# Kernel tuning notes

Hardware: AMD Instinct MI355X
Metric: run time of the kernel (lower is better)

The kernel has to match this reference:

```python
import jax, jax.numpy as jnp
import numpy as np

B, T, V, EMB, KBD, H, NF, OUT = 256, 50, 100000, 64, 64, 128, 10, 64


def setup_inputs() -> dict:
    key = jax.random.key(0)
    ks = jax.random.split(key, 18)
    s = 0.05
    f = lambda i, shape: jax.random.normal(ks[i], shape, jnp.float32) * s
    return {
        "X": jax.random.randint(ks[0], (B, T), 0, V),
        "E": f(1, (V, EMB)),
        "KBE": f(2, (V, KBD)),
        "r_matrix": f(3, (NF, KBD)),
        "gru_Wih": f(4, (3 * H, EMB)),
        "gru_Whh": f(5, (3 * H, H)),
        "gru_bih": f(6, (3 * H,)),
        "gru_bhh": f(7, (3 * H,)),
        "u_W": f(8, (KBD, H)),
        "u_b": f(9, (KBD,)),
        "ea_W": f(10, (KBD, KBD)),
        "ea_b": f(11, (KBD,)),
        "u2_W": f(12, (H, KBD + H)),
        "u2_b": f(13, (H,)),
        "m1_W": f(14, (OUT, H)),
        "m1_b": f(15, (OUT,)),
        "m2_W": f(16, (OUT, EMB + KBD)),
        "m2_b": f(17, (OUT,)),
    }


def reference(X, E, KBE, r_matrix, gru_Wih, gru_Whh, gru_bih, gru_bhh,
              u_W, u_b, ea_W, ea_b, u2_W, u2_b, m1_W, m1_b, m2_W, m2_b):
    b, t = X.shape
    nf, d = r_matrix.shape
    hdim = gru_Whh.shape[1]
    # mask row 0 of the embedding tables (padding item)
    Em = E.at[0].set(0.0)
    KBEm = KBE.at[0].set(0.0)
    Sx = Em[X]        # [B,T,EMB]
    KBx = KBEm[X]     # [B,T,KBD]

    h0 = jnp.zeros((b, hdim), Sx.dtype)
    MN0 = jnp.zeros((b, nf, d), Sx.dtype)
    ysum0 = jnp.zeros((b, m1_b.shape[0]), Sx.dtype)

    def step(carry, xs):
        h, MN, ysum = carry
        x_emb, kb = xs
        # torch GRUCell
        gi = x_emb @ gru_Wih.T + gru_bih
        gh = h @ gru_Whh.T + gru_bhh
        ir, iz, inn = jnp.split(gi, 3, axis=1)
        hr, hz, hn = jnp.split(gh, 3, axis=1)
        r = jax.nn.sigmoid(ir + hr)
        z = jax.nn.sigmoid(iz + hz)
        n = jnp.tanh(inn + r * hn)
        h = (1.0 - z) * n + z * h
        # memory write
        EA = jnp.tanh(kb @ ea_W.T + ea_b)[:, None, :] + r_matrix      # [B,NF,D]
        gate = jax.nn.sigmoid(jnp.sum(MN * EA, axis=-1, keepdims=True))  # [B,NF,1]
        MN = MN * (1.0 - gate) + EA * gate
        # memory read
        U = jnp.tanh(h @ u_W.T + u_b)                                  # [B,D]
        AW = jax.nn.softmax(U @ r_matrix.T, axis=1)                    # [B,NF]
        AC = jnp.einsum('bnd,bn->bd', MN, AW)                          # [B,D]
        Ut = jnp.tanh(jnp.concatenate([h, AC], axis=-1) @ u2_W.T + u2_b)
        y = jnp.tanh(Ut @ m1_W.T + m1_b)                               # [B,OUT]
        return (h, MN, ysum + y), None

    (h, MN, ysum), _ = jax.lax.scan(
        step, (h0, MN0, ysum0),
        (Sx.transpose(1, 0, 2), KBx.transpose(1, 0, 2)))
    y = ysum / t

    MergeE = jnp.concatenate([E, KBE], axis=1).at[0].set(0.0)  # [V, EMB+KBD]
    Sy = jnp.tanh(MergeE @ m2_W.T + m2_b)                      # [V, OUT]
    return jax.nn.log_softmax(y @ Sy.T, axis=1)                # [B, V]
```

## Files before the change

kernel.cpp:

```cpp
#include <hip/hip_runtime.h>
#include <hip/hip_bf16.h>
#include <math.h>

#define BB 256
#define TT 50
#define VV 100000
#define EMB 64
#define KBD 64
#define HH 128
#define NF 10
#define OUTD 64
#define G3H 384
#define NTILE 6250
#define DSTR 16
#define NSY 240

typedef __attribute__((ext_vector_type(8))) short sh8;
typedef __attribute__((ext_vector_type(4))) short sh4;
typedef __attribute__((ext_vector_type(4))) float f32x4;

__device__ __forceinline__ float frcp(float x){ return __builtin_amdgcn_rcpf(x); }
__device__ __forceinline__ float sigm(float x){ return frcp(1.0f+__expf(-x)); }
__device__ __forceinline__ float tanhf_(float x){ return 1.0f - 2.0f*frcp(__expf(2.0f*x)+1.0f); }
__device__ __forceinline__ short f2bs(float f){ __hip_bfloat16 h=__float2bfloat16(f); return *reinterpret_cast<short*>(&h); }
__device__ __forceinline__ sh8 ldfrag(const float* p){
  float4 a = *(const float4*)p; float4 b = *(const float4*)(p+4);
  sh8 v;
  v[0]=f2bs(a.x); v[1]=f2bs(a.y); v[2]=f2bs(a.z); v[3]=f2bs(a.w);
  v[4]=f2bs(b.x); v[5]=f2bs(b.y); v[6]=f2bs(b.z); v[7]=f2bs(b.w);
  return v;
}
__device__ __forceinline__ void barrier_lds(){
  asm volatile("s_waitcnt lgkmcnt(0)" ::: "memory");
  __builtin_amdgcn_sched_barrier(0);
  __builtin_amdgcn_s_barrier();
  __builtin_amdgcn_sched_barrier(0);
}

__global__ void k_trans(const float* __restrict__ Wih, const float* __restrict__ eaW,
                        float* __restrict__ WihT, float* __restrict__ eaWT) {
  int stride = gridDim.x*blockDim.x;
  int tid0 = blockIdx.x*blockDim.x + threadIdx.x;
  for (int i=tid0; i<G3H*EMB; i+=stride){ int j=i/EMB, k=i%EMB; WihT[k*G3H+j]=Wih[i]; }
  for (int i=tid0; i<KBD*KBD; i+=stride){ int j=i/KBD, k=i%KBD; eaWT[k*KBD+j]=eaW[i]; }
}

#define PREP 32
__global__ __launch_bounds__(512) void k_preSy(
    const int* __restrict__ X, const float* __restrict__ E, const float* __restrict__ KBE,
    const float* __restrict__ WihT, const float* __restrict__ bih, const float* __restrict__ bhh,
    const float* __restrict__ eaWT, const float* __restrict__ eab,
    float* __restrict__ gi_pre, float* __restrict__ ea_pre,
    __hip_bfloat16* __restrict__ ea_bfT,
    const float* __restrict__ m2W, const float* __restrict__ m2b,
    __hip_bfloat16* __restrict__ Sy) {
  const int tid = threadIdx.x;
  const int w = tid>>6, l = tid&63, r16 = l&15, g4 = l>>4;

  if (blockIdx.x >= 400) {
    int kof = g4*8;
    sh8 bbf[4][4];
    float bias[4];
    #pragma unroll
    for (int nt=0;nt<4;nt++){
      int o = nt*16 + r16;
      bias[nt] = m2b[o];
      #pragma unroll
      for (int ks=0;ks<4;ks++) bbf[nt][ks] = ldfrag(m2W + o*128 + ks*32 + kof);
    }
    int wid = (blockIdx.x-400)*8 + w;
    for (int tile=wid; tile<NTILE; tile+=NSY*8){
      int v = tile*16 + r16;
      sh8 aa[4];
      const float* ep = E + (size_t)v*EMB + kof;
      const float* kp = KBE + (size_t)v*KBD + kof;
      aa[0] = ldfrag(ep); aa[1] = ldfrag(ep+32);
      aa[2] = ldfrag(kp); aa[3] = ldfrag(kp+32);
      if (v==0){ sh8 z={0,0,0,0,0,0,0,0}; aa[0]=z;aa[1]=z;aa[2]=z;aa[3]=z; }
      f32x4 acc[4];
      #pragma unroll
      for (int nt=0;nt<4;nt++){ f32x4 z={0.f,0.f,0.f,0.f}; acc[nt]=z; }
      #pragma unroll
      for (int nt=0;nt<4;nt++)
        #pragma unroll
        for (int ks=0;ks<4;ks++)
          acc[nt] = __builtin_amdgcn_mfma_f32_16x16x32_bf16(aa[ks],bbf[nt][ks],acc[nt],0,0,0);
      #pragma unroll
      for (int nt=0;nt<4;nt++){
        #pragma unroll
        for (int r=0;r<4;r++){
          int vv = tile*16 + g4*4 + r;
          Sy[(size_t)vv*OUTD + nt*16 + r16] = __float2bfloat16(tanhf_(acc[nt][r] + bias[nt]));
        }
      }
    }
    return;
  }

  __shared__ float xeL[PREP][EMB];
  __shared__ float kbL[PREP][KBD];
  int base = blockIdx.x * PREP;
  for (int i=tid; i<PREP*EMB; i+=512){
    int p=i>>6, k=i&63; int x = X[base+p];
    xeL[p][k] = x ? E[(size_t)x*EMB+k] : 0.0f;
    kbL[p][k] = x ? KBE[(size_t)x*KBD+k] : 0.0f;
  }
  __syncthreads();
  if (tid < G3H) {
    int j = tid;
    float acc[PREP];
    #pragma unroll
    for (int p=0;p<PREP;p++) acc[p]=0.f;
    for (int k=0;k<EMB;k++){
      float ww = WihT[k*G3H+j];
      #pragma unroll
      for (int p=0;p<PREP;p++) acc[p] += ww*xeL[p][k];
    }
    float bj = bih[j] + (j < 2*HH ? bhh[j] : 0.0f);
    for (int p=0;p<PREP;p++) gi_pre[((size_t)(base+p))*G3H + j] = acc[p]+bj;
  }
  {
    int d = tid & 63; int pg = tid >> 6;
    float bd = eab[d];
    for (int p=pg; p<PREP; p+=8){
      float acc=0.f;
      #pragma unroll 8
      for (int k=0;k<KBD;k++) acc += eaWT[k*KBD+d]*kbL[p][k];
      float v = tanhf(acc + bd);
      int pair = base+p;
      int bb = pair/TT, tt = pair - bb*TT;
      ea_pre[((size_t)pair)*KBD + d] = v;
      ea_bfT[((size_t)bb*64 + d)*64 + tt] = __float2bfloat16(v);
    }
  }
}

__global__ __launch_bounds__(256,2) void k_scanh(
    const float* __restrict__ gi_pre,
    const float* __restrict__ Whh, const float* __restrict__ bhh,
    const float* __restrict__ ea_pre, const float* __restrict__ rmat,
    float* __restrict__ Gg, float* __restrict__ Pg,
    __hip_bfloat16* __restrict__ h_stream) {
  const int tid = threadIdx.x;
  const int w = tid>>6, l = tid&63, r16 = l&15, g4 = l>>4;

  if (blockIdx.x >= 16) {
    const int b = (blockIdx.x-16)*4 + w;
    sh8 aa[4][2];
    #pragma unroll
    for (int i=0;i<4;i++){
      int row = i*16 + r16; if (row > TT-1) row = TT-1;
      #pragma unroll
      for (int f=0;f<2;f++)
        aa[i][f] = ldfrag(ea_pre + ((size_t)b*TT + row)*KBD + f*32 + g4*8);
    }
    sh8 rmB[2];
    #pragma unroll
    for (int f=0;f<2;f++){
      sh8 z = {0,0,0,0,0,0,0,0};
      if (r16 < NF) z = ldfrag(rmat + (size_t)r16*KBD + f*32 + g4*8);
      rmB[f] = z;
    }
    float* Gb = Gg + ((size_t)b<<12);
    #pragma unroll
    for (int i=0;i<4;i++){
      #pragma unroll
      for (int j=0;j<4;j++){
        f32x4 acc={0.f,0.f,0.f,0.f};
        #pragma unroll
        for (int f=0;f<2;f++) acc = __builtin_amdgcn_mfma_f32_16x16x32_bf16(aa[i][f], aa[j][f], acc,0,0,0);
        #pragma unroll
        for (int r=0;r<4;r++) Gb[(i*16+g4*4+r)*64 + j*16+r16] = acc[r];
      }
      f32x4 accp={0.f,0.f,0.f,0.f};
      #pragma unroll
      for (int f=0;f<2;f++) accp = __builtin_amdgcn_mfma_f32_16x16x32_bf16(aa[i][f], rmB[f], accp,0,0,0);
      #pragma unroll
      for (int r=0;r<4;r++) Pg[((size_t)b<<10) + (i*16+g4*4+r)*16 + r16] = accp[r];
    }
    return;
  }

  __shared__ __hip_bfloat16 hcat[2][16][128];
  __builtin_amdgcn_s_setprio(1);
  const int b = blockIdx.x;
  const int b0 = b*16;
  for (int i=tid;i<2*16*128;i+=256) ((short*)hcat)[i]=0;
  __syncthreads();
  const int swz = (r16&7)<<4;

  sh8 whhF[2][3][4];
  #pragma unroll
  for (int t=0;t<2;t++)
    #pragma unroll
    for (int g=0;g<3;g++){
      int chain = (w + 4*t) + 8*g;
      #pragma unroll
      for (int f=0;f<4;f++)
        whhF[t][g][f] = ldfrag(Whh + (size_t)(chain*16 + r16)*HH + f*32 + g4*8);
    }
  float4 bhn[2];
  bhn[0] = *(const float4*)(bhh + 2*HH + w*16 + g4*4);
  bhn[1] = *(const float4*)(bhh + 2*HH + (w+4)*16 + g4*4);
  float h_old[2][4] = {{0.f,0.f,0.f,0.f},{0.f,0.f,0.f,0.f}};
  const float* gi_row = gi_pre + (size_t)(b0+r16)*TT*G3H;
  __hip_bfloat16* hsb = h_stream + (size_t)b*TT*16*HH;

  int cur = 0;
  auto stepfn = [&](int s, float4 (&gi)[2][3], int cu){
    const char* hrow = (const char*)&hcat[cu][r16][0];
    sh8 hb[4];
    #pragma unroll
    for (int f=0;f<4;f++)
      hb[f] = *(const sh8*)(hrow + ((f*64 + g4*16) ^ swz));
    f32x4 aR[2], aZ[2], aN[2];
    #pragma unroll
    for (int t=0;t<2;t++){ f32x4 z={0.f,0.f,0.f,0.f}; aR[t]=z; aZ[t]=z; aN[t]=z; }
    #pragma unroll
    for (int f=0;f<4;f++){
      #pragma unroll
      for (int t=0;t<2;t++){
        aR[t] = __builtin_amdgcn_mfma_f32_16x16x32_bf16(whhF[t][0][f], hb[f], aR[t],0,0,0);
        aZ[t] = __builtin_amdgcn_mfma_f32_16x16x32_bf16(whhF[t][1][f], hb[f], aZ[t],0,0,0);
        aN[t] = __builtin_amdgcn_mfma_f32_16x16x32_bf16(whhF[t][2][f], hb[f], aN[t],0,0,0);
      }
    }
    char* hwrow = (char*)&hcat[cu^1][r16][0];
    #pragma unroll
    for (int t=0;t<2;t++){
      sh4 hp;
      #pragma unroll
      for (int r=0;r<4;r++){
        float rr = sigm(gi[t][0][r] + aR[t][r]);
        float zz = sigm(gi[t][1][r] + aZ[t][r]);
        float nn = tanhf_(gi[t][2][r] + rr*(aN[t][r] + bhn[t][r]));
        h_old[t][r] = (1.f-zz)*nn + zz*h_old[t][r];
        hp[r] = f2bs(h_old[t][r]);
      }
      *(sh4*)(hwrow + (((w+4*t)*32 + g4*8) ^ swz)) = hp;
      *(sh4*)(hsb + ((size_t)s*16 + r16)*HH + (w+4*t)*16 + g4*4) = hp;
    }
    barrier_lds();
  };

  float4 gA[2][3], gB[2][3];
  #pragma unroll
  for (int t=0;t<2;t++)
    #pragma unroll
    for (int g=0;g<3;g++)
      gA[t][g] = *(const float4*)(gi_row + g*128 + (w+4*t)*16 + g4*4);

  for (int s=0;s<TT;s+=2){
    {
      int sg = s+1;
      #pragma unroll
      for (int t=0;t<2;t++)
        #pragma unroll
        for (int g=0;g<3;g++)
          gB[t][g] = *(const float4*)(gi_row + (size_t)sg*G3H + g*128 + (w+4*t)*16 + g4*4);
      stepfn(s, gA, cur);
      cur ^= 1;
    }
    {
      int sg = (s+2<TT)? s+2 : TT-1;
      #pragma unroll
      for (int t=0;t<2;t++)
        #pragma unroll
        for (int g=0;g<3;g++)
          gA[t][g] = *(const float4*)(gi_row + (size_t)sg*G3H + g*128 + (w+4*t)*16 + g4*4);
      stepfn(s+1, gB, cur);
      cur ^= 1;
    }
  }
}

__global__ __launch_bounds__(512) void k_uaw(
    const __hip_bfloat16* __restrict__ h_stream,
    const float* __restrict__ uW, const float* __restrict__ ub,
    const float* __restrict__ rmat, float* __restrict__ aw_pre) {
  __shared__ __hip_bfloat16 u_sh[8][16][72];
  const int tid = threadIdx.x;
  const int w = tid>>6, l = tid&63, r16 = l&15, g4 = l>>4;
  sh8 uwF[4][4];
  #pragma unroll
  for (int ot=0;ot<4;ot++)
    #pragma unroll
    for (int f=0;f<4;f++)
      uwF[ot][f] = ldfrag(uW + (size_t)(ot*16+r16)*HH + f*32 + g4*8);
  sh8 rmF[2];
  #pragma unroll
  for (int f=0;f<2;f++){
    sh8 z = {0,0,0,0,0,0,0,0};
    if (r16 < NF) z = ldfrag(rmat + (size_t)r16*KBD + f*32 + g4*8);
    rmF[f] = z;
  }
  float4 ubv[4];
  #pragma unroll
  for (int ot=0;ot<4;ot++) ubv[ot] = *(const float4*)(ub + ot*16 + g4*4);

  int p0 = (blockIdx.x*8 + w)*16;
  int t = p0>>8, b0 = p0&255, fb = b0>>4;
  const __hip_bfloat16* hp = h_stream + (size_t)((fb*TT + t)*16)*HH;
  sh8 hb[4];
  #pragma unroll
  for (int f=0;f<4;f++) hb[f] = *(const sh8*)(hp + r16*HH + f*32 + g4*8);
  f32x4 u[4];
  #pragma unroll
  for (int ot=0;ot<4;ot++){ f32x4 z={0.f,0.f,0.f,0.f}; u[ot]=z; }
  #pragma unroll
  for (int ot=0;ot<4;ot++)
    #pragma unroll
    for (int f=0;f<4;f++)
      u[ot] = __builtin_amdgcn_mfma_f32_16x16x32_bf16(uwF[ot][f], hb[f], u[ot],0,0,0);
  #pragma unroll
  for (int ot=0;ot<4;ot++){
    sh4 up;
    #pragma unroll
    for (int r=0;r<4;r++) up[r] = f2bs(tanhf_(u[ot][r] + ubv[ot][r]));
    *(sh4*)&u_sh[w][l&15][ot*16 + g4*4] = up;
  }
  __syncthreads();
  sh8 uf[2];
  #pragma unroll
  for (int f=0;f<2;f++) uf[f] = *(const sh8*)&u_sh[w][r16][f*32 + g4*8];
  f32x4 al={0.f,0.f,0.f,0.f};
  #pragma unroll
  for (int f=0;f<2;f++) al = __builtin_amdgcn_mfma_f32_16x16x32_bf16(rmF[f], uf[f], al,0,0,0);
  float mx = -1e30f;
  #pragma unroll
  for (int r=0;r<4;r++){ if (g4*4+r < NF) mx = fmaxf(mx, al[r]); }
  mx = fmaxf(mx, __shfl_xor(mx,16));
  mx = fmaxf(mx, __shfl_xor(mx,32));
  float av[4]; float ssum=0.f;
  #pragma unroll
  for (int r=0;r<4;r++){ av[r] = (g4*4+r < NF) ? __expf(al[r]-mx) : 0.f; ssum += av[r]; }
  ssum += __shfl_xor(ssum,16); ssum += __shfl_xor(ssum,32);
  float inv = frcp(ssum);
  if (g4<3){
    f32x4 o = {av[0]*inv, av[1]*inv, av[2]*inv, av[3]*inv};
    *(f32x4*)&aw_pre[(size_t)(p0+r16)*16 + g4*4] = o;
  }
}

__global__ __launch_bounds__(640) void k_mnrec(
    const float* __restrict__ Gg, const float* __restrict__ Pg,
    const float* __restrict__ rmat, const float* __restrict__ aw_pre,
    __hip_bfloat16* __restrict__ Aag_bf, __hip_bfloat16* __restrict__ Bag_bf) {
  __shared__ float AagL[TT*52];
  __shared__ float BagL[TT*16];
  const int tid = threadIdx.x;
  const int n = tid>>6, l = tid&63;
  const int b = blockIdx.x;
  for (int i=tid;i<TT*52;i+=640) AagL[i]=0.f;
  for (int i=tid;i<TT*16;i+=640) BagL[i]=0.f;

  float rv = rmat[n*KBD + l];
  float R = rv*rv;
  R += __shfl_xor(R,1); R += __shfl_xor(R,2); R += __shfl_xor(R,4);
  R += __shfl_xor(R,8); R += __shfl_xor(R,16); R += __shfl_xor(R,32);

  float Pn = (l<TT)? Pg[((size_t)b<<10) + l*16 + n] : 0.f;
  const float* Gb = Gg + ((size_t)b<<12);
  float Grow = Gb[l];
  float awt = aw_pre[(size_t)(0*256+b)*16 + n];
  float d=0.f, w=0.f, q=1.f;
  __syncthreads();

  for (int t=0;t<TT;t++){
    int tn = (t+1<TT)? t+1 : TT-1;
    float GrowN = Gb[tn*64 + l];
    float awtN  = aw_pre[(size_t)(tn*256+b)*16 + n];
    float dt = __shfl(d, t);
    float g  = sigm(dt);
    float og = 1.f - g;
    float Pt = __shfl(Pn, t);
    float Ets = Grow + Pt + Pn + R;
    d = og*d + g*Ets;
    w = (l==t)? g : w*og;
    q *= og;
    if (l < TT) atomicAdd(&AagL[t*52 + l], awt*w);
    if (l == 0) BagL[t*16 + n] = awt*(1.f - q);
    Grow = GrowN; awt = awtN;
  }
  __syncthreads();
  for (int i=tid;i<4096;i+=640){
    int row=i>>6, col=i&63;
    float v = (row<TT && col<TT)? AagL[row*52+col] : 0.f;
    Aag_bf[((size_t)b<<12) + i] = __float2bfloat16(v);
  }
  for (int i=tid;i<2048;i+=640){
    int row=i>>5, col=i&31;
    float v = (row<TT && col<NF)? BagL[row*16+col] : 0.f;
    Bag_bf[((size_t)b<<11) + i] = __float2bfloat16(v);
  }
}

__global__ __launch_bounds__(512) void k_ac(
    const __hip_bfloat16* __restrict__ Aag_bf, const __hip_bfloat16* __restrict__ Bag_bf,
    const __hip_bfloat16* __restrict__ ea_bfT, const float* __restrict__ rmat,
    __hip_bfloat16* __restrict__ ac_pre) {
  const int tid = threadIdx.x;
  const int w = tid>>6, l = tid&63, r16 = l&15, g4 = l>>4;
  const int b = blockIdx.x*8 + w;
  sh8 a1[4][2], a2[4];
  #pragma unroll
  for (int i=0;i<4;i++){
    #pragma unroll
    for (int f=0;f<2;f++)
      a1[i][f] = *(const sh8*)(Aag_bf + ((size_t)b<<12) + (i*16+r16)*64 + f*32 + g4*8);
    a2[i] = *(const sh8*)(Bag_bf + ((size_t)b<<11) + (i*16+r16)*32 + g4*8);
  }
  for (int j=0;j<4;j++){
    sh8 bb1[2];
    #pragma unroll
    for (int f=0;f<2;f++)
      bb1[f] = *(const sh8*)(ea_bfT + ((size_t)b<<12) + (j*16+r16)*64 + f*32 + g4*8);
    sh8 bb2;
    #pragma unroll
    for (int c=0;c<8;c++){
      int k = g4*8 + c;
      bb2[c] = (k<NF)? f2bs(rmat[k*KBD + j*16+r16]) : (short)0;
    }
    #pragma unroll
    for (int i=0;i<4;i++){
      f32x4 acc={0.f,0.f,0.f,0.f};
      #pragma unroll
      for (int f=0;f<2;f++) acc = __builtin_amdgcn_mfma_f32_16x16x32_bf16(a1[i][f], bb1[f], acc,0,0,0);
      acc = __builtin_amdgcn_mfma_f32_16x16x32_bf16(a2[i], bb2, acc,0,0,0);
      #pragma unroll
      for (int r=0;r<4;r++){
        int t = i*16 + g4*4 + r;
        if (t < TT)
          ac_pre[((size_t)t*256 + b)*KBD + j*16 + r16] = __float2bfloat16(acc[r]);
      }
    }
  }
}

__global__ __launch_bounds__(512) void k_uty(
    const __hip_bfloat16* __restrict__ h_stream, const __hip_bfloat16* __restrict__ ac_pre,
    const float* __restrict__ u2W, const float* __restrict__ u2b,
    const float* __restrict__ m1W, const float* __restrict__ m1b,
    __hip_bfloat16* __restrict__ y_tmp) {
  __shared__ __hip_bfloat16 ut_sh[16][136];
  const int tid = threadIdx.x;
  const int w = tid>>6, l = tid&63, r16 = l&15, g4 = l>>4;
  const int t = blockIdx.x>>4, btile = blockIdx.x&15;
  const int b0 = btile*16, fb = btile;

  sh8 u2F[6];
  #pragma unroll
  for (int f=0;f<6;f++) u2F[f] = ldfrag(u2W + (size_t)(w*16+r16)*(HH+KBD) + f*32 + g4*8);
  sh8 m1F[4];
  if (w<4){
    #pragma unroll
    for (int f=0;f<4;f++) m1F[f] = ldfrag(m1W + (size_t)(w*16+r16)*HH + f*32 + g4*8);
  }
  float4 u2bv = *(const float4*)(u2b + w*16 + g4*4);

  const __hip_bfloat16* hp = h_stream + (size_t)((fb*TT + t)*16)*HH;
  const __hip_bfloat16* ap = ac_pre + ((size_t)t*256 + b0)*KBD;
  sh8 cb[6];
  #pragma unroll
  for (int f=0;f<4;f++) cb[f] = *(const sh8*)(hp + r16*HH + f*32 + g4*8);
  #pragma unroll
  for (int f=4;f<6;f++) cb[f] = *(const sh8*)(ap + r16*KBD + (f-4)*32 + g4*8);
  f32x4 at={0.f,0.f,0.f,0.f};
  #pragma unroll
  for (int f=0;f<6;f++) at = __builtin_amdgcn_mfma_f32_16x16x32_bf16(u2F[f], cb[f], at,0,0,0);
  sh4 tp;
  #pragma unroll
  for (int r=0;r<4;r++) tp[r] = f2bs(tanhf_(at[r] + u2bv[r]));
  *(sh4*)&ut_sh[r16][w*16+g4*4] = tp;
  __syncthreads();
  if (w<4){
    float4 m1bv = *(const float4*)(m1b + w*16 + g4*4);
    sh8 tb[4];
    #pragma unroll
    for (int f=0;f<4;f++) tb[f] = *(const sh8*)&ut_sh[r16][f*32+g4*8];
    f32x4 ay={0.f,0.f,0.f,0.f};
    #pragma unroll
    for (int f=0;f<4;f++) ay = __builtin_amdgcn_mfma_f32_16x16x32_bf16(m1F[f], tb[f], ay,0,0,0);
    sh4 yp;
    #pragma unroll
    for (int r=0;r<4;r++) yp[r] = f2bs(tanhf_(ay[r] + m1bv[r]));
    *(sh4*)&y_tmp[((size_t)t*256 + b0 + r16)*OUTD + w*16 + g4*4] = yp;
  }
}

__global__ __launch_bounds__(512) void k_fin(
    const __hip_bfloat16* __restrict__ y_tmp, __hip_bfloat16* __restrict__ ybf) {
  int idx = blockIdx.x*512 + threadIdx.x;
  int b = idx>>6, o = idx&63;
  float s = 0.f;
  for (int t=0;t<TT;t++) s += __bfloat162float(y_tmp[((size_t)t*256 + b)*OUTD + o]);
  ybf[(size_t)b*OUTD + o] = __float2bfloat16(s*(1.0f/TT));
}

__global__ __launch_bounds__(256) void k_logits(
    const __hip_bfloat16* __restrict__ ybf, const __hip_bfloat16* __restrict__ Sy,
    float* __restrict__ denom, float* __restrict__ out, int pass) {
  __shared__ float dsum[64];
  int lane = threadIdx.x & 63;
  int w = threadIdx.x >> 6;
  int r16 = lane & 15, g4 = lane >> 4;
  int kof = g4 * 8;
  int tbase = blockIdx.x * 16 + w * 4;
  if (pass==0){
    if (threadIdx.x<64) dsum[threadIdx.x]=0.f;
    __syncthreads();
  }
  sh8 b0[4], b1[4];
  #pragma unroll
  for (int i=0;i<4;i++){
    if (tbase + i < NTILE) {
      const __hip_bfloat16* bp = Sy + ((size_t)((tbase+i)*16 + r16))*OUTD + kof;
      b0[i] = *(const sh8*)bp;
      b1[i] = *(const sh8*)(bp + 32);
    } else {
      sh8 z = {0,0,0,0,0,0,0,0};
      b0[i]=z; b1[i]=z;
    }
  }
  int bg0 = blockIdx.y * 4;
  for (int bgi=0; bgi<4; bgi++){
    int bg = bg0 + bgi;
    const __hip_bfloat16* ap = ybf + (bg*16 + r16)*OUTD + kof;
    sh8 a0 = *(const sh8*)ap;
    sh8 a1 = *(const sh8*)(ap+32);
    if (pass == 0){
      float part[4] = {0.f,0.f,0.f,0.f};
      #pragma unroll
      for (int i=0;i<4;i++){
        if (tbase + i < NTILE){
          f32x4 acc = {0.f,0.f,0.f,0.f};
          acc = __builtin_amdgcn_mfma_f32_16x16x32_bf16(a0,b0[i],acc,0,0,0);
          acc = __builtin_amdgcn_mfma_f32_16x16x32_bf16(a1,b1[i],acc,0,0,0);
          #pragma unroll
          for (int r=0;r<4;r++) part[r] += __expf(acc[r]);
        }
      }
      #pragma unroll
      for (int r=0;r<4;r++){
        float p = part[r];
        p += __shfl_xor(p,1,16); p += __shfl_xor(p,2,16);
        p += __shfl_xor(p,4,16); p += __shfl_xor(p,8,16);
        if (r16==0) atomicAdd(&dsum[bgi*16 + g4*4 + r], p);
      }
    } else {
      float lse[4];
      #pragma unroll
      for (int r=0;r<4;r++) lse[r] = logf(denom[(size_t)(bg*16 + g4*4 + r)*DSTR]);
      #pragma unroll
      for (int i=0;i<4;i++){
        if (tbase + i < NTILE){
          f32x4 acc = {0.f,0.f,0.f,0.f};
          acc = __builtin_amdgcn_mfma_f32_16x16x32_bf16(a0,b0[i],acc,0,0,0);
          acc = __builtin_amdgcn_mfma_f32_16x16x32_bf16(a1,b1[i],acc,0,0,0);
          int vc = (tbase+i)*16 + r16;
          #pragma unroll
          for (int r=0;r<4;r++)
            out[(size_t)(bg*16 + g4*4 + r)*VV + vc] = acc[r] - lse[r];
        }
      }
    }
  }
  if (pass==0){
    __syncthreads();
    if (threadIdx.x<64)
      atomicAdd(&denom[(size_t)(bg0*16 + threadIdx.x)*DSTR], dsum[threadIdx.x]);
  }
}

extern "C" void kernel_launch(void* const* d_in, const int* in_sizes, int n_in,
                              void* d_out, int out_size, void* d_ws, size_t ws_size,
                              hipStream_t stream) {
  const int*   X    = (const int*)  d_in[0];
  const float* E    = (const float*)d_in[1];
  const float* KBE  = (const float*)d_in[2];
  const float* rmat = (const float*)d_in[3];
  const float* Wih  = (const float*)d_in[4];
  const float* Whh  = (const float*)d_in[5];
  const float* bih  = (const float*)d_in[6];
  const float* bhh  = (const float*)d_in[7];
  const float* uW   = (const float*)d_in[8];
  const float* ub   = (const float*)d_in[9];
  const float* eaW  = (const float*)d_in[10];
  const float* eab  = (const float*)d_in[11];
  const float* u2W  = (const float*)d_in[12];
  const float* u2b  = (const float*)d_in[13];
  const float* m1W  = (const float*)d_in[14];
  const float* m1b  = (const float*)d_in[15];
  const float* m2W  = (const float*)d_in[16];
  const float* m2b  = (const float*)d_in[17];
  float* outp = (float*)d_out;

  char* p = (char*)d_ws;
  float* WihT   = (float*)p;            p += (size_t)EMB*G3H*4;
  float* eaWT   = (float*)p;            p += (size_t)KBD*KBD*4;
  float* gi_pre = (float*)p;            p += (size_t)BB*TT*G3H*4;
  float* ea_pre = (float*)p;            p += (size_t)BB*TT*KBD*4;
  float* denom  = (float*)p;            p += (size_t)BB*DSTR*4;
  float* aw_pre = (float*)p;            p += (size_t)BB*TT*16*4;
  float* Gg     = (float*)p;            p += (size_t)BB*64*64*4;
  float* Pg     = (float*)p;            p += (size_t)BB*64*16*4;
  __hip_bfloat16* h_stream = (__hip_bfloat16*)p; p += (size_t)16*TT*16*HH*2;
  __hip_bfloat16* ea_bfT = (__hip_bfloat16*)p;   p += (size_t)BB*64*64*2;
  __hip_bfloat16* Aag_bf = (__hip_bfloat16*)p;   p += (size_t)BB*64*64*2;
  __hip_bfloat16* Bag_bf = (__hip_bfloat16*)p;   p += (size_t)BB*64*32*2;
  __hip_bfloat16* ac_pre = (__hip_bfloat16*)p;   p += (size_t)BB*TT*KBD*2;
  __hip_bfloat16* y_tmp  = (__hip_bfloat16*)p;   p += (size_t)BB*TT*OUTD*2;
  __hip_bfloat16* ybf    = (__hip_bfloat16*)p;   p += (size_t)BB*OUTD*2;
  __hip_bfloat16* Sy     = (__hip_bfloat16*)p;   p += (size_t)VV*OUTD*2;

  k_trans<<<32,256,0,stream>>>(Wih,eaW,WihT,eaWT);
  hipMemsetAsync(denom, 0, BB*DSTR*sizeof(float), stream);
  k_preSy<<<400+NSY,512,0,stream>>>(X,E,KBE,WihT,bih,bhh,eaWT,eab,gi_pre,ea_pre,ea_bfT,
                                    m2W,m2b,Sy);
  k_scanh<<<80,256,0,stream>>>(gi_pre,Whh,bhh,ea_pre,rmat,Gg,Pg,h_stream);
  k_uaw<<<100,512,0,stream>>>(h_stream,uW,ub,rmat,aw_pre);
  k_mnrec<<<256,640,0,stream>>>(Gg,Pg,rmat,aw_pre,Aag_bf,Bag_bf);
  k_ac<<<32,512,0,stream>>>(Aag_bf,Bag_bf,ea_bfT,rmat,ac_pre);
  k_uty<<<TT*16,512,0,stream>>>(h_stream,ac_pre,u2W,u2b,m1W,m1b,y_tmp);
  k_fin<<<32,512,0,stream>>>(y_tmp,ybf);
  dim3 g1((NTILE + 15)/16, 4, 1);
  k_logits<<<g1,256,0,stream>>>(ybf,Sy,denom,outp,0);
  k_logits<<<g1,256,0,stream>>>(ybf,Sy,denom,outp,1);
}
```

Measured before the change: 264.3 us.

## Use bf16 MFMA for input-gate and erase projections, drop transpose kernel

```diff
diff --git a/kernel.cpp b/kernel.cpp
--- a/kernel.cpp
+++ b/kernel.cpp
@@ -37,19 +37,11 @@
   __builtin_amdgcn_sched_barrier(0);
 }
 
-__global__ void k_trans(const float* __restrict__ Wih, const float* __restrict__ eaW,
-                        float* __restrict__ WihT, float* __restrict__ eaWT) {
-  int stride = gridDim.x*blockDim.x;
-  int tid0 = blockIdx.x*blockDim.x + threadIdx.x;
-  for (int i=tid0; i<G3H*EMB; i+=stride){ int j=i/EMB, k=i%EMB; WihT[k*G3H+j]=Wih[i]; }
-  for (int i=tid0; i<KBD*KBD; i+=stride){ int j=i/KBD, k=i%KBD; eaWT[k*KBD+j]=eaW[i]; }
-}
-
 #define PREP 32
 __global__ __launch_bounds__(512) void k_preSy(
     const int* __restrict__ X, const float* __restrict__ E, const float* __restrict__ KBE,
-    const float* __restrict__ WihT, const float* __restrict__ bih, const float* __restrict__ bhh,
-    const float* __restrict__ eaWT, const float* __restrict__ eab,
+    const float* __restrict__ Wih, const float* __restrict__ bih, const float* __restrict__ bhh,
+    const float* __restrict__ eaW, const float* __restrict__ eab,
     float* __restrict__ gi_pre, float* __restrict__ ea_pre,
     __hip_bfloat16* __restrict__ ea_bfT,
     const float* __restrict__ m2W, const float* __restrict__ m2b,
@@ -97,8 +89,8 @@
     return;
   }
 
-  __shared__ float xeL[PREP][EMB];
-  __shared__ float kbL[PREP][KBD];
+  __shared__ float xeL[PREP][68];
+  __shared__ float kbL[PREP][68];
   int base = blockIdx.x * PREP;
   for (int i=tid; i<PREP*EMB; i+=512){
     int p=i>>6, k=i&63; int x = X[base+p];
@@ -106,30 +98,44 @@
     kbL[p][k] = x ? KBE[(size_t)x*KBD+k] : 0.0f;
   }
   __syncthreads();
-  if (tid < G3H) {
-    int j = tid;
-    float acc[PREP];
-    #pragma unroll
-    for (int p=0;p<PREP;p++) acc[p]=0.f;
-    for (int k=0;k<EMB;k++){
-      float ww = WihT[k*G3H+j];
-      #pragma unroll
-      for (int p=0;p<PREP;p++) acc[p] += ww*xeL[p][k];
-    }
+
+  const int m = w>>2, nq = w&3;
+  sh8 axe[2], akb[2];
+  #pragma unroll
+  for (int f=0;f<2;f++){
+    axe[f] = ldfrag(&xeL[m*16 + r16][f*32 + g4*8]);
+    akb[f] = ldfrag(&kbL[m*16 + r16][f*32 + g4*8]);
+  }
+  #pragma unroll
+  for (int i=0;i<6;i++){
+    int nt = nq*6 + i;
+    int j = nt*16 + r16;
+    sh8 bf0 = ldfrag(Wih + (size_t)j*EMB + g4*8);
+    sh8 bf1 = ldfrag(Wih + (size_t)j*EMB + 32 + g4*8);
+    f32x4 acc = {0.f,0.f,0.f,0.f};
+    acc = __builtin_amdgcn_mfma_f32_16x16x32_bf16(axe[0], bf0, acc,0,0,0);
+    acc = __builtin_amdgcn_mfma_f32_16x16x32_bf16(axe[1], bf1, acc,0,0,0);
     float bj = bih[j] + (j < 2*HH ? bhh[j] : 0.0f);
-    for (int p=0;p<PREP;p++) gi_pre[((size_t)(base+p))*G3H + j] = acc[p]+bj;
+    #pragma unroll
+    for (int r=0;r<4;r++){
+      int pair = base + m*16 + g4*4 + r;
+      gi_pre[(size_t)pair*G3H + j] = acc[r] + bj;
+    }
   }
   {
-    int d = tid & 63; int pg = tid >> 6;
+    int d = nq*16 + r16;
+    sh8 bf0 = ldfrag(eaW + (size_t)d*KBD + g4*8);
+    sh8 bf1 = ldfrag(eaW + (size_t)d*KBD + 32 + g4*8);
+    f32x4 acc = {0.f,0.f,0.f,0.f};
+    acc = __builtin_amdgcn_mfma_f32_16x16x32_bf16(akb[0], bf0, acc,0,0,0);
+    acc = __builtin_amdgcn_mfma_f32_16x16x32_bf16(akb[1], bf1, acc,0,0,0);
     float bd = eab[d];
-    for (int p=pg; p<PREP; p+=8){
-      float acc=0.f;
-      #pragma unroll 8
-      for (int k=0;k<KBD;k++) acc += eaWT[k*KBD+d]*kbL[p][k];
-      float v = tanhf(acc + bd);
-      int pair = base+p;
+    #pragma unroll
+    for (int r=0;r<4;r++){
+      int pair = base + m*16 + g4*4 + r;
+      float v = tanhf(acc[r] + bd);
+      ea_pre[(size_t)pair*KBD + d] = v;
       int bb = pair/TT, tt = pair - bb*TT;
-      ea_pre[((size_t)pair)*KBD + d] = v;
       ea_bfT[((size_t)bb*64 + d)*64 + tt] = __float2bfloat16(v);
     }
   }
@@ -596,8 +602,6 @@
   float* outp = (float*)d_out;
 
   char* p = (char*)d_ws;
-  float* WihT   = (float*)p;            p += (size_t)EMB*G3H*4;
-  float* eaWT   = (float*)p;            p += (size_t)KBD*KBD*4;
   float* gi_pre = (float*)p;            p += (size_t)BB*TT*G3H*4;
   float* ea_pre = (float*)p;            p += (size_t)BB*TT*KBD*4;
   float* denom  = (float*)p;            p += (size_t)BB*DSTR*4;
@@ -613,9 +617,8 @@
   __hip_bfloat16* ybf    = (__hip_bfloat16*)p;   p += (size_t)BB*OUTD*2;
   __hip_bfloat16* Sy     = (__hip_bfloat16*)p;   p += (size_t)VV*OUTD*2;
 
-  k_trans<<<32,256,0,stream>>>(Wih,eaW,WihT,eaWT);
   hipMemsetAsync(denom, 0, BB*DSTR*sizeof(float), stream);
-  k_preSy<<<400+NSY,512,0,stream>>>(X,E,KBE,WihT,bih,bhh,eaWT,eab,gi_pre,ea_pre,ea_bfT,
+  k_preSy<<<400+NSY,512,0,stream>>>(X,E,KBE,Wih,bih,bhh,eaW,eab,gi_pre,ea_pre,ea_bfT,
                                     m2W,m2b,Sy);
   k_scanh<<<80,256,0,stream>>>(gi_pre,Whh,bhh,ea_pre,rmat,Gg,Pg,h_stream);
   k_uaw<<<100,512,0,stream>>>(h_stream,uW,ub,rmat,aw_pre);
```

Result: faster. 240.4 us (-9.0%).
